# Optimization experiments

Hardware: AMD Instinct MI355X
Metric: run time of the kernel (lower is better)

The kernel has to match this reference:

```python
import jax, jax.numpy as jnp
import numpy as np


def setup_inputs() -> dict:
    key = jax.random.key(0)
    k1, k2, k3 = jax.random.split(key, 3)
    B, C, Q, E = 32, 2048, 128, 200
    x_contexts = jax.random.normal(k1, (B, C, E), dtype=jnp.float32)
    x_questions = jax.random.normal(k2, (B, Q, E), dtype=jnp.float32)
    # weight of nn.Linear(3E, 1, bias=False), flattened to (3E,)
    w_sim = jax.random.normal(k3, (3 * E,), dtype=jnp.float32) * (1.0 / np.sqrt(3 * E))
    return {"x_contexts": x_contexts, "x_questions": x_questions, "w_sim": w_sim}


def reference(x_contexts, x_questions, w_sim):
    # x_contexts: [B,C,E], x_questions: [B,Q,E], w_sim: [3E]
    E = x_contexts.shape[-1]
    w1, w2, w3 = w_sim[:E], w_sim[E:2 * E], w_sim[2 * E:]
    # Trilinear similarity S[b,c,q] = w1.c + w2.q + w3.(c*q), decomposed so the
    # [B,C,Q,3E] tensor of the original expand+cat+linear is never materialized.
    s_c = jnp.einsum('bce,e->bc', x_contexts, w1)              # [B,C]
    s_q = jnp.einsum('bqe,e->bq', x_questions, w2)             # [B,Q]
    s_cq = jnp.einsum('bce,bqe->bcq', x_contexts * w3, x_questions)  # [B,C,Q]
    S = s_cq + s_c[:, :, None] + s_q[:, None, :]               # [B,C,Q]

    # Context-to-question: row softmax over Q, then attend over questions.
    c2q = jnp.einsum('bcq,bqe->bce', jax.nn.softmax(S, axis=-1), x_questions)

    # Question-to-context: max over Q, softmax over C, attend over contexts.
    q2c_w = jax.nn.softmax(jnp.max(S, axis=-1), axis=-1)       # [B,C]
    q2c = jnp.einsum('bc,bce->be', q2c_w, x_contexts)          # [B,E]
    q2c = q2c[:, None, :]                                      # broadcast to [B,C,E]

    return jnp.concatenate(
        [x_contexts, c2q, x_contexts * c2q, x_contexts * q2c], axis=-1)  # [B,C,4E]
```

## Files before the change

kernel.cpp:

```cpp
#include <hip/hip_runtime.h>

#define B_ 32
#define C_ 2048
#define Q_ 128
#define E_ 200
#define TB 32

typedef __attribute__((ext_vector_type(4))) float f32x4;

__global__ __launch_bounds__(256) void prep_kernel(const float* __restrict__ xq,
                                                   const float* __restrict__ w,
                                                   float* __restrict__ xqT,
                                                   float* __restrict__ sq) {
    __shared__ float tl[32][33];
    if (blockIdx.x < 896) {
        const int blk = blockIdx.x;
        const int b  = blk / 28;
        const int r  = blk - b * 28;
        const int qt = r / 7, et = r - (r / 7) * 7;
        const int q0 = qt * 32, e0 = et * 32;
        const int tx = threadIdx.x & 31, ty = threadIdx.x >> 5;
        #pragma unroll
        for (int i = 0; i < 4; ++i) {
            const int q = q0 + ty + 8 * i, e = e0 + tx;
            if (e < E_) tl[ty + 8 * i][tx] = xq[((size_t)b * Q_ + q) * E_ + e];
        }
        __syncthreads();
        #pragma unroll
        for (int i = 0; i < 4; ++i) {
            const int e = e0 + ty + 8 * i, q = q0 + tx;
            if (e < E_) xqT[((size_t)b * E_ + e) * Q_ + q] = tl[tx][ty + 8 * i];
        }
    } else {
        const int wave = (blockIdx.x - 896) * 4 + (threadIdx.x >> 6);
        const int lane = threadIdx.x & 63;
        const float* row = xq + (size_t)wave * E_;
        float a = 0.f;
        if (lane < 50) {
            const f32x4 v  = *(const f32x4*)&row[lane * 4];
            const f32x4 wv = *(const f32x4*)&w[E_ + lane * 4];
            a = (v.x * wv.x + v.y * wv.y) + (v.z * wv.z + v.w * wv.w);
        }
        #pragma unroll
        for (int off = 32; off; off >>= 1) a += __shfl_xor(a, off);
        if (lane == 0) sq[wave] = a;
    }
}

__global__ __launch_bounds__(256) void row2_kernel(const float* __restrict__ xc_g,
                                                   const float* __restrict__ xq_g,
                                                   const float* __restrict__ xqT_g,
                                                   const float* __restrict__ w_g,
                                                   const float* __restrict__ sq_g,
                                                   float* __restrict__ m_g,
                                                   float* __restrict__ out) {
    __shared__ float scw3_l[TB][E_];
    __shared__ float P_l[TB][Q_];
    __shared__ float sc_l[TB];

    const int t    = threadIdx.x;
    const int blk  = blockIdx.x;
    const int x    = blk & 7;
    const int g    = blk >> 3;
    const int b    = x * 4 + (g >> 6);
    const int tile = g & 63;
    const int bc0  = b * C_ + tile * TB;

    {
        const int r  = t >> 3;
        const int k  = t & 7;
        const int e0 = k * 25;
        const float* xc_row = xc_g + (size_t)(bc0 + r) * E_;
        float p1 = 0.f;
        #pragma unroll
        for (int i = 0; i < 25; ++i) {
            const int e = e0 + i;
            const float v = xc_row[e];
            scw3_l[r][e] = v * w_g[2 * E_ + e];
            p1 = fmaf(v, w_g[e], p1);
        }
        p1 += __shfl_xor(p1, 1);
        p1 += __shfl_xor(p1, 2);
        p1 += __shfl_xor(p1, 4);
        if (k == 0) sc_l[r] = p1;
    }
    __syncthreads();

    const int qg = t & 31;
    const int cg = t >> 5;
    const int c4 = cg * 4;
    const int q4 = qg * 4;

    f32x4 acc[4] = {};
    const float* xqT_b = xqT_g + (size_t)b * E_ * Q_;
    for (int e = 0; e < E_; e += 4) {
        const f32x4 x0 = *(const f32x4*)&xqT_b[(e + 0) * Q_ + q4];
        const f32x4 x1 = *(const f32x4*)&xqT_b[(e + 1) * Q_ + q4];
        const f32x4 x2 = *(const f32x4*)&xqT_b[(e + 2) * Q_ + q4];
        const f32x4 x3 = *(const f32x4*)&xqT_b[(e + 3) * Q_ + q4];
        #pragma unroll
        for (int ci = 0; ci < 4; ++ci) {
            const f32x4 a = *(const f32x4*)&scw3_l[c4 + ci][e];
            acc[ci] += a.x * x0 + a.y * x1 + a.z * x2 + a.w * x3;
        }
    }

    const f32x4 sqv = *(const f32x4*)&sq_g[b * Q_ + q4];
    float mx[4], sm[4];
    #pragma unroll
    for (int ci = 0; ci < 4; ++ci) {
        acc[ci] += sc_l[c4 + ci] + sqv;
        mx[ci] = fmaxf(fmaxf(acc[ci].x, acc[ci].y), fmaxf(acc[ci].z, acc[ci].w));
    }
    #pragma unroll
    for (int off = 16; off; off >>= 1) {
        #pragma unroll
        for (int ci = 0; ci < 4; ++ci) mx[ci] = fmaxf(mx[ci], __shfl_xor(mx[ci], off));
    }
    if (qg == 0) {
        #pragma unroll
        for (int ci = 0; ci < 4; ++ci) m_g[bc0 + c4 + ci] = mx[ci];
    }
    #pragma unroll
    for (int ci = 0; ci < 4; ++ci) {
        f32x4 p;
        p.x = __expf(acc[ci].x - mx[ci]);
        p.y = __expf(acc[ci].y - mx[ci]);
        p.z = __expf(acc[ci].z - mx[ci]);
        p.w = __expf(acc[ci].w - mx[ci]);
        acc[ci] = p;
        sm[ci] = (p.x + p.y) + (p.z + p.w);
    }
    #pragma unroll
    for (int off = 16; off; off >>= 1) {
        #pragma unroll
        for (int ci = 0; ci < 4; ++ci) sm[ci] += __shfl_xor(sm[ci], off);
    }
    #pragma unroll
    for (int ci = 0; ci < 4; ++ci) {
        acc[ci] *= (1.f / sm[ci]);
        *(f32x4*)&P_l[c4 + ci][q4] = acc[ci];
    }
    __syncthreads();

    const float* xq_b = xq_g + (size_t)b * Q_ * E_;
    #pragma unroll
    for (int pass = 0; pass < 2; ++pass) {
        const int e4 = pass * 128 + q4;
        if (e4 < E_) {
            f32x4 o[4] = {};
            for (int q = 0; q < Q_; q += 4) {
                const f32x4 xv0 = *(const f32x4*)&xq_b[(q + 0) * E_ + e4];
                const f32x4 xv1 = *(const f32x4*)&xq_b[(q + 1) * E_ + e4];
                const f32x4 xv2 = *(const f32x4*)&xq_b[(q + 2) * E_ + e4];
                const f32x4 xv3 = *(const f32x4*)&xq_b[(q + 3) * E_ + e4];
                #pragma unroll
                for (int ci = 0; ci < 4; ++ci) {
                    const f32x4 p = *(const f32x4*)&P_l[c4 + ci][q];
                    o[ci] += p.x * xv0 + p.y * xv1 + p.z * xv2 + p.w * xv3;
                }
            }
            #pragma unroll
            for (int ci = 0; ci < 4; ++ci) {
                const size_t row = (size_t)(bc0 + c4 + ci);
                const f32x4 xcv = *(const f32x4*)&xc_g[row * E_ + e4];
                float* orow = out + row * (4 * E_);
                *(f32x4*)&orow[e4]          = xcv;
                *(f32x4*)&orow[E_ + e4]     = o[ci];
                *(f32x4*)&orow[2 * E_ + e4] = xcv * o[ci];
            }
        }
    }
}

__global__ __launch_bounds__(256) void q2c_partial(const float* __restrict__ xc_g,
                                                   const float* __restrict__ m_g,
                                                   float* __restrict__ part,
                                                   float* __restrict__ den) {
    __shared__ float redl[4];
    __shared__ float wl[64];
    const int blk = blockIdx.x;
    const int b = blk >> 5, g = blk & 31;
    const int t = threadIdx.x;
    const int c0 = g * 64;

    float mx = -3.4e38f;
    #pragma unroll
    for (int j = 0; j < 8; ++j) mx = fmaxf(mx, m_g[b * C_ + t + j * 256]);
    #pragma unroll
    for (int off = 32; off; off >>= 1) mx = fmaxf(mx, __shfl_xor(mx, off));
    if ((t & 63) == 0) redl[t >> 6] = mx;
    __syncthreads();
    const float M = fmaxf(fmaxf(redl[0], redl[1]), fmaxf(redl[2], redl[3]));

    if (t < 64) {
        const float e = __expf(m_g[b * C_ + c0 + t] - M);
        wl[t] = e;
        float s = e;
        #pragma unroll
        for (int off = 32; off; off >>= 1) s += __shfl_xor(s, off);
        if (t == 0) den[blk] = s;
    }
    __syncthreads();

    if (t < E_) {
        float acc = 0.f;
        const float* base = xc_g + ((size_t)(b * C_ + c0)) * E_ + t;
        #pragma unroll 8
        for (int c = 0; c < 64; ++c) acc = fmaf(wl[c], base[(size_t)c * E_], acc);
        part[(size_t)blk * E_ + t] = acc;
    }
}

__global__ __launch_bounds__(256) void out4_kernel(const float* __restrict__ xc_g,
                                                   const float* __restrict__ part,
                                                   const float* __restrict__ den,
                                                   float* __restrict__ out) {
    __shared__ float q2c_l[E_];
    __shared__ float invt;
    const int blk = blockIdx.x;
    const int b = blk >> 5, g = blk & 31;
    const int c0 = g * 64;
    const int t = threadIdx.x;

    if (t < E_) {
        float a = 0.f;
        #pragma unroll
        for (int gg = 0; gg < 32; ++gg) a += part[(size_t)(b * 32 + gg) * E_ + t];
        q2c_l[t] = a;
    }
    if (t >= 224) {
        float s = den[b * 32 + (t - 224)];
        #pragma unroll
        for (int off = 16; off; off >>= 1) s += __shfl_xor(s, off);
        if (t == 224) invt = 1.f / s;
    }
    __syncthreads();

    const float iv = invt;
    const int e4 = (t % 50) * 4;
    const int r0 = t / 50;
    if (t < 200) {
        #pragma unroll
        for (int kk = 0; kk < 16; ++kk) {
            const size_t row = (size_t)(b * C_ + c0 + kk * 4 + r0);
            const f32x4 xcv = *(const f32x4*)&xc_g[row * E_ + e4];
            const f32x4 qv  = *(const f32x4*)&q2c_l[e4];
            *(f32x4*)&out[row * (4 * E_) + 3 * E_ + e4] = xcv * (qv * iv);
        }
    }
}

extern "C" void kernel_launch(void* const* d_in, const int* in_sizes, int n_in,
                              void* d_out, int out_size, void* d_ws, size_t ws_size,
                              hipStream_t stream) {
    const float* xc = (const float*)d_in[0];
    const float* xq = (const float*)d_in[1];
    const float* w  = (const float*)d_in[2];
    for (int i = 0; i < n_in; ++i) {
        if      (in_sizes[i] == B_ * C_ * E_) xc = (const float*)d_in[i];
        else if (in_sizes[i] == B_ * Q_ * E_) xq = (const float*)d_in[i];
        else if (in_sizes[i] == 3 * E_)       w  = (const float*)d_in[i];
    }
    float* out = (float*)d_out;

    float* ws    = (float*)d_ws;
    float* sq    = ws;
    float* m     = sq + B_ * Q_;
    float* xqT   = m + B_ * C_;
    float* part  = xqT;
    float* den   = xqT + 1024 * E_;

    prep_kernel <<<1920,               256, 0, stream>>>(xq, w, xqT, sq);
    row2_kernel <<<B_ * (C_ / TB),     256, 0, stream>>>(xc, xq, xqT, w, sq, m, out);
    q2c_partial <<<B_ * 32,            256, 0, stream>>>(xc, m, part, den);
    out4_kernel <<<B_ * 32,            256, 0, stream>>>(xc, part, den, out);
}
```

Before: 395.2 us.

## Halve softmax-probability LDS buffer and fuse both E passes into one Q loop

The row kernel's shared probability tile now holds only 64 of the 128 question columns. It is filled in two phases separated by barriers, which cuts LDS use per block. The two separate E-column passes are merged into one loop over Q that updates both accumulator sets, so each P read from LDS is reused for both halves. This may allow more blocks per CU, but it adds two barriers, doubles the accumulator registers, and leaves the act_b half of the threads idle.

After: 402.5 us. Within noise of the previous version (+1.9%).

```diff
diff --git a/kernel.cpp b/kernel.cpp
--- a/kernel.cpp
+++ b/kernel.cpp
@@ -55,7 +55,7 @@
                                                    float* __restrict__ m_g,
                                                    float* __restrict__ out) {
     __shared__ float scw3_l[TB][E_];
-    __shared__ float P_l[TB][Q_];
+    __shared__ float P_h[TB][64];
     __shared__ float sc_l[TB];
 
     const int t    = threadIdx.x;
@@ -137,38 +137,77 @@
         for (int ci = 0; ci < 4; ++ci) sm[ci] += __shfl_xor(sm[ci], off);
     }
     #pragma unroll
+    for (int ci = 0; ci < 4; ++ci) acc[ci] *= (1.f / sm[ci]);
+
+    const float* xq_b = xq_g + (size_t)b * Q_ * E_;
+    const int e4a = q4;
+    const int e4b = 128 + q4;
+    const bool act_b = (e4b < E_);
+    f32x4 oa[4] = {}, ob[4] = {};
+
+    if (qg < 16) {
+        #pragma unroll
+        for (int ci = 0; ci < 4; ++ci) *(f32x4*)&P_h[c4 + ci][q4] = acc[ci];
+    }
+    __syncthreads();
+    for (int q = 0; q < 64; q += 4) {
+        const f32x4 v0 = *(const f32x4*)&xq_b[(q + 0) * E_ + e4a];
+        const f32x4 v1 = *(const f32x4*)&xq_b[(q + 1) * E_ + e4a];
+        const f32x4 v2 = *(const f32x4*)&xq_b[(q + 2) * E_ + e4a];
+        const f32x4 v3 = *(const f32x4*)&xq_b[(q + 3) * E_ + e4a];
+        f32x4 w0, w1, w2, w3;
+        if (act_b) {
+            w0 = *(const f32x4*)&xq_b[(q + 0) * E_ + e4b];
+            w1 = *(const f32x4*)&xq_b[(q + 1) * E_ + e4b];
+            w2 = *(const f32x4*)&xq_b[(q + 2) * E_ + e4b];
+            w3 = *(const f32x4*)&xq_b[(q + 3) * E_ + e4b];
+        }
+        #pragma unroll
+        for (int ci = 0; ci < 4; ++ci) {
+            const f32x4 p = *(const f32x4*)&P_h[c4 + ci][q];
+            oa[ci] += p.x * v0 + p.y * v1 + p.z * v2 + p.w * v3;
+            if (act_b) ob[ci] += p.x * w0 + p.y * w1 + p.z * w2 + p.w * w3;
+        }
+    }
+    __syncthreads();
+    if (qg >= 16) {
+        #pragma unroll
+        for (int ci = 0; ci < 4; ++ci) *(f32x4*)&P_h[c4 + ci][q4 - 64] = acc[ci];
+    }
+    __syncthreads();
+    for (int q = 64; q < Q_; q += 4) {
+        const f32x4 v0 = *(const f32x4*)&xq_b[(q + 0) * E_ + e4a];
+        const f32x4 v1 = *(const f32x4*)&xq_b[(q + 1) * E_ + e4a];
+        const f32x4 v2 = *(const f32x4*)&xq_b[(q + 2) * E_ + e4a];
+        const f32x4 v3 = *(const f32x4*)&xq_b[(q + 3) * E_ + e4a];
+        f32x4 w0, w1, w2, w3;
+        if (act_b) {
+            w0 = *(const f32x4*)&xq_b[(q + 0) * E_ + e4b];
+            w1 = *(const f32x4*)&xq_b[(q + 1) * E_ + e4b];
+            w2 = *(const f32x4*)&xq_b[(q + 2) * E_ + e4b];
+            w3 = *(const f32x4*)&xq_b[(q + 3) * E_ + e4b];
+        }
+        #pragma unroll
+        for (int ci = 0; ci < 4; ++ci) {
+            const f32x4 p = *(const f32x4*)&P_h[c4 + ci][q - 64];
+            oa[ci] += p.x * v0 + p.y * v1 + p.z * v2 + p.w * v3;
+            if (act_b) ob[ci] += p.x * w0 + p.y * w1 + p.z * w2 + p.w * w3;
+        }
+    }
+
+    #pragma unroll
     for (int ci = 0; ci < 4; ++ci) {
-        acc[ci] *= (1.f / sm[ci]);
-        *(f32x4*)&P_l[c4 + ci][q4] = acc[ci];
-    }
-    __syncthreads();
-
-    const float* xq_b = xq_g + (size_t)b * Q_ * E_;
-    #pragma unroll
-    for (int pass = 0; pass < 2; ++pass) {
-        const int e4 = pass * 128 + q4;
-        if (e4 < E_) {
-            f32x4 o[4] = {};
-            for (int q = 0; q < Q_; q += 4) {
-                const f32x4 xv0 = *(const f32x4*)&xq_b[(q + 0) * E_ + e4];
-                const f32x4 xv1 = *(const f32x4*)&xq_b[(q + 1) * E_ + e4];
-                const f32x4 xv2 = *(const f32x4*)&xq_b[(q + 2) * E_ + e4];
-                const f32x4 xv3 = *(const f32x4*)&xq_b[(q + 3) * E_ + e4];
-                #pragma unroll
-                for (int ci = 0; ci < 4; ++ci) {
-                    const f32x4 p = *(const f32x4*)&P_l[c4 + ci][q];
-                    o[ci] += p.x * xv0 + p.y * xv1 + p.z * xv2 + p.w * xv3;
-                }
-            }
-            #pragma unroll
-            for (int ci = 0; ci < 4; ++ci) {
-                const size_t row = (size_t)(bc0 + c4 + ci);
-                const f32x4 xcv = *(const f32x4*)&xc_g[row * E_ + e4];
-                float* orow = out + row * (4 * E_);
-                *(f32x4*)&orow[e4]          = xcv;
-                *(f32x4*)&orow[E_ + e4]     = o[ci];
-                *(f32x4*)&orow[2 * E_ + e4] = xcv * o[ci];
-            }
+        const size_t row = (size_t)(bc0 + c4 + ci);
+        float* orow = out + row * (4 * E_);
+        const f32x4 xa = *(const f32x4*)&xc_g[row * E_ + e4a];
+        *(f32x4*)&orow[e4a]          = xa;
+        *(f32x4*)&orow[E_ + e4a]     = oa[ci];
+        *(f32x4*)&orow[2 * E_ + e4a] = xa * oa[ci];
+        if (act_b) {
+            const f32x4 xb = *(const f32x4*)&xc_g[row * E_ + e4b];
+            *(f32x4*)&orow[e4b]          = xb;
+            *(f32x4*)&orow[E_ + e4b]     = ob[ci];
+            *(f32x4*)&orow[2 * E_ + e4b] = xb * ob[ci];
         }
     }
 }
```
